# Kernel optimization log

Measured on AMD Instinct MI355X. Metric: run time of the kernel, lower is better.

Reference implementation:

```python
import jax, jax.numpy as jnp
import numpy as np

ALPHA = 0.2  # leaky relu negative slope
F_DIM = 128  # n_features


def setup_inputs() -> dict:
    key = jax.random.key(0)
    k1, k2, k3, k4 = jax.random.split(key, 4)
    B, K, F = 4, 256, F_DIM
    E2 = 2 * F  # embed_dim*2 == 2*n_features (embed_dim defaults to n_features)
    x = jax.random.normal(k1, (B, K, F), dtype=jnp.float32)
    # nn.Linear(2F, 2E): weight (out=2E, in=2F), bias (2E,)
    W = jax.random.normal(k2, (E2, 2 * F), dtype=jnp.float32) * np.sqrt(2.0 / (E2 + 2 * F))
    b_lin = jnp.zeros((E2,), dtype=jnp.float32)
    # attention vector a: xavier_uniform with gain 1.414 on shape (2E, 1)
    limit = 1.414 * np.sqrt(6.0 / (E2 + 1))
    a = jax.random.uniform(k3, (E2,), dtype=jnp.float32, minval=-limit, maxval=limit)
    bias = jnp.zeros((K, K), dtype=jnp.float32)
    return {"x": x, "W": W, "b_lin": b_lin, "a": a, "bias": bias}


def reference(x, W, b_lin, a, bias):
    # Faithful math: combined[b,i,j] = cat(x[b,i], x[b,j]); lin is linear, so
    # lin(cat(vi,vj)) = vi @ W1^T + vj @ W2^T + b  with W = [W1 | W2] split on input dim.
    F = x.shape[-1]
    W1, W2 = W[:, :F], W[:, F:]              # each (2E, F)
    s1 = jnp.einsum('bkf,ef->bke', x, W1)     # contribution of the 'query' time step i
    s2 = jnp.einsum('bkf,ef->bke', x, W2)     # contribution of the 'key' time step j
    pre = s1[:, :, None, :] + s2[:, None, :, :] + b_lin  # (B,K,K,2E)
    h = jnp.where(pre >= 0, pre, ALPHA * pre)            # leaky_relu
    e = jnp.einsum('bije,e->bij', h, a) + bias           # (B,K,K)
    attn = jax.nn.softmax(e, axis=2)
    # dropout with train=False is identity (module evaluated in eval mode)
    out = jax.nn.sigmoid(jnp.einsum('bij,bjf->bif', attn, x))  # (B,K,F)
    return out
```

## Files before the change

### kernel.cpp

```cpp
#include <hip/hip_runtime.h>

#define ALPHA 0.2f
constexpr int B  = 4;
constexpr int K  = 256;
constexpr int F  = 128;
constexpr int E2 = 256;
constexpr int ET = 512;

__global__ __launch_bounds__(256) void k1_gemm(const float* __restrict__ x,
                                               const float* __restrict__ W,
                                               const float* __restrict__ bl,
                                               float* __restrict__ S) {
    __shared__ float xt[32][132];
    __shared__ float wt[64][132];
    const int b  = blockIdx.z;
    const int k0 = blockIdx.y * 32;
    const int e0 = blockIdx.x * 64;
    const int tid = threadIdx.x;

    const int col4 = (tid & 31) * 4;
    const int rsub = tid >> 5;
#pragma unroll
    for (int p = 0; p < 4; ++p) {
        int row = p * 8 + rsub;
        *(float4*)&xt[row][col4] =
            *(const float4*)&x[(b * K + k0 + row) * F + col4];
    }
#pragma unroll
    for (int p = 0; p < 8; ++p) {
        int row = p * 8 + rsub;
        int eg  = e0 + row;
        int wr  = eg & (E2 - 1);
        int fb  = (eg >= E2) ? F : 0;
        *(float4*)&wt[row][col4] =
            *(const float4*)&W[wr * (2 * F) + fb + col4];
    }
    __syncthreads();

    const int es = tid & 15;
    const int kb = tid >> 4;
    float acc[2][4] = {};
    for (int f4 = 0; f4 < F; f4 += 4) {
        float4 x0 = *(const float4*)&xt[kb][f4];
        float4 x1 = *(const float4*)&xt[kb + 16][f4];
#pragma unroll
        for (int t = 0; t < 4; ++t) {
            float4 wv = *(const float4*)&wt[es + 16 * t][f4];
            acc[0][t] += x0.x * wv.x + x0.y * wv.y + x0.z * wv.z + x0.w * wv.w;
            acc[1][t] += x1.x * wv.x + x1.y * wv.y + x1.z * wv.z + x1.w * wv.w;
        }
    }

    const bool isS2 = (e0 >= E2);
#pragma unroll
    for (int t = 0; t < 4; ++t) {
        int   eg  = e0 + es + 16 * t;
        float add = isS2 ? bl[eg - E2] : 0.f;
#pragma unroll
        for (int kk = 0; kk < 2; ++kk) {
            int kg = k0 + kb + 16 * kk;
            S[(b * K + kg) * ET + eg] = acc[kk][t] + add;
        }
    }
}

__global__ __launch_bounds__(256) void k2_score(const float* __restrict__ S,
                                                const float* __restrict__ a,
                                                const float* __restrict__ bias,
                                                float* __restrict__ Eo) {
    __shared__ float s1t[16][260];
    __shared__ float s2t[32][260];
    __shared__ float av6[256];
    __shared__ float av4[256];
    const int b  = blockIdx.z;
    const int i0 = blockIdx.y * 16;
    const int j0 = blockIdx.x * 32;
    const int tid = threadIdx.x;

    { float av = a[tid]; av6[tid] = 0.6f * av; av4[tid] = 0.4f * av; }

    const int col4 = (tid & 63) * 4;
    const int rsub = tid >> 6;
#pragma unroll
    for (int p = 0; p < 4; ++p) {
        int row = p * 4 + rsub;
        *(float4*)&s1t[row][col4] =
            *(const float4*)&S[(b * K + i0 + row) * ET + col4];
    }
#pragma unroll
    for (int p = 0; p < 8; ++p) {
        int row = p * 4 + rsub;
        *(float4*)&s2t[row][col4] =
            *(const float4*)&S[(b * K + j0 + row) * ET + E2 + col4];
    }
    __syncthreads();

    const int w    = tid >> 6;
    const int lane = tid & 63;
    const int jl   = lane & 31;
    const int eh   = lane >> 5;
    float acc[4] = {0.f, 0.f, 0.f, 0.f};
    const int ebeg = eh * 128;

#pragma unroll 2
    for (int e = ebeg; e < ebeg + 128; e += 4) {
        float4 sv = *(const float4*)&s2t[jl][e];
        float4 c6 = *(const float4*)&av6[e];
        float4 c4 = *(const float4*)&av4[e];
#pragma unroll
        for (int is = 0; is < 4; ++is) {
            float4 s1v = *(const float4*)&s1t[w * 4 + is][e];
            float p0 = s1v.x + sv.x;
            float p1 = s1v.y + sv.y;
            float p2 = s1v.z + sv.z;
            float p3 = s1v.w + sv.w;
            acc[is] += c6.x * p0 + c4.x * fabsf(p0);
            acc[is] += c6.y * p1 + c4.y * fabsf(p1);
            acc[is] += c6.z * p2 + c4.z * fabsf(p2);
            acc[is] += c6.w * p3 + c4.w * fabsf(p3);
        }
    }
#pragma unroll
    for (int is = 0; is < 4; ++is) acc[is] += __shfl_xor(acc[is], 32);

    if (eh == 0) {
        int jg = j0 + jl;
#pragma unroll
        for (int is = 0; is < 4; ++is) {
            int ig = i0 + w * 4 + is;
            Eo[(b * K + ig) * K + jg] = acc[is] + bias[ig * K + jg];
        }
    }
}

__global__ __launch_bounds__(256) void k3_softmax_pv(const float* __restrict__ Ein,
                                                     const float* __restrict__ x,
                                                     float* __restrict__ out) {
    __shared__ float p_lds[K][4];
    __shared__ float yp[4][4][F];
    __shared__ float rinv_lds[4];
    const int b   = blockIdx.y;
    const int i0  = blockIdx.x * 4;
    const int tid = threadIdx.x;
    const int w   = tid >> 6;
    const int lane = tid & 63;

    const int i = i0 + w;
    const float* Erow = &Ein[(b * K + i) * K];
    float er[4];
#pragma unroll
    for (int m = 0; m < 4; ++m) er[m] = Erow[m * 64 + lane];
    float mx = fmaxf(fmaxf(er[0], er[1]), fmaxf(er[2], er[3]));
#pragma unroll
    for (int off = 32; off > 0; off >>= 1) mx = fmaxf(mx, __shfl_xor(mx, off));
    float pm[4], s = 0.f;
#pragma unroll
    for (int m = 0; m < 4; ++m) { pm[m] = __expf(er[m] - mx); s += pm[m]; }
#pragma unroll
    for (int off = 32; off > 0; off >>= 1) s += __shfl_xor(s, off);
    if (lane == 0) rinv_lds[w] = 1.f / s;
#pragma unroll
    for (int m = 0; m < 4; ++m) p_lds[m * 64 + lane][w] = pm[m];
    __syncthreads();

    float acc[4][2] = {};
    const float* xb = &x[(size_t)(b * K) * F];
#pragma unroll 4
    for (int jj = 0; jj < 64; ++jj) {
        int j = w * 64 + jj;
        float2 xv = *(const float2*)&xb[j * F + lane * 2];
        float4 pj = *(const float4*)&p_lds[j][0];
        acc[0][0] += pj.x * xv.x;  acc[0][1] += pj.x * xv.y;
        acc[1][0] += pj.y * xv.x;  acc[1][1] += pj.y * xv.y;
        acc[2][0] += pj.z * xv.x;  acc[2][1] += pj.z * xv.y;
        acc[3][0] += pj.w * xv.x;  acc[3][1] += pj.w * xv.y;
    }
#pragma unroll
    for (int ii = 0; ii < 4; ++ii) {
        yp[w][ii][lane * 2]     = acc[ii][0];
        yp[w][ii][lane * 2 + 1] = acc[ii][1];
    }
    __syncthreads();

#pragma unroll
    for (int r = 0; r < 2; ++r) {
        int id = r * 256 + tid;
        int ii = id >> 7;
        int f  = id & 127;
        float y = yp[0][ii][f] + yp[1][ii][f] + yp[2][ii][f] + yp[3][ii][f];
        float z = y * rinv_lds[ii];
        out[(b * K + i0 + ii) * F + f] = 1.f / (1.f + __expf(-z));
    }
}

extern "C" void kernel_launch(void* const* d_in, const int* in_sizes, int n_in,
                              void* d_out, int out_size, void* d_ws, size_t ws_size,
                              hipStream_t stream) {
    const float* x    = (const float*)d_in[0];
    const float* W    = (const float*)d_in[1];
    const float* bl   = (const float*)d_in[2];
    const float* a    = (const float*)d_in[3];
    const float* bias = (const float*)d_in[4];
    float* out = (float*)d_out;

    float* S = (float*)d_ws;
    float* E = (float*)((char*)d_ws + (size_t)B * K * ET * sizeof(float));

    k1_gemm      <<<dim3(ET / 64, K / 32, B), 256, 0, stream>>>(x, W, bl, S);
    k2_score     <<<dim3(K / 32, K / 16, B), 256, 0, stream>>>(S, a, bias, E);
    k3_softmax_pv<<<dim3(K / 4, B),          256, 0, stream>>>(E, x, out);
}
```

Before: 29.29 us.

## Fuse score computation with softmax and PV, shrink GEMM tile for more blocks

The score kernel and the softmax/PV kernel are merged, so each block of 4 query rows computes its full 256-wide score row in registers and LDS, streaming S2 tiles through double-buffered shared memory. This removes the intermediate E buffer round trip through global memory and one kernel launch. The GEMM tile along E is halved so the first kernel launches twice as many blocks. In exchange, each fused block rereads all of S2 for its batch, and per-block LDS grows (about 90 KB), which limits occupancy. The fused grid is only 256 blocks.

Result: slower. 36.90 us (+26.0%).

```diff
diff --git a/kernel.cpp b/kernel.cpp
--- a/kernel.cpp
+++ b/kernel.cpp
@@ -1,6 +1,5 @@
 #include <hip/hip_runtime.h>
 
-#define ALPHA 0.2f
 constexpr int B  = 4;
 constexpr int K  = 256;
 constexpr int F  = 128;
@@ -12,10 +11,10 @@
                                                const float* __restrict__ bl,
                                                float* __restrict__ S) {
     __shared__ float xt[32][132];
-    __shared__ float wt[64][132];
+    __shared__ float wt[32][132];
     const int b  = blockIdx.z;
     const int k0 = blockIdx.y * 32;
-    const int e0 = blockIdx.x * 64;
+    const int e0 = blockIdx.x * 32;
     const int tid = threadIdx.x;
 
     const int col4 = (tid & 31) * 4;
@@ -25,13 +24,9 @@
         int row = p * 8 + rsub;
         *(float4*)&xt[row][col4] =
             *(const float4*)&x[(b * K + k0 + row) * F + col4];
-    }
-#pragma unroll
-    for (int p = 0; p < 8; ++p) {
-        int row = p * 8 + rsub;
-        int eg  = e0 + row;
-        int wr  = eg & (E2 - 1);
-        int fb  = (eg >= E2) ? F : 0;
+        int eg = e0 + row;
+        int wr = eg & (E2 - 1);
+        int fb = (eg >= E2) ? F : 0;
         *(float4*)&wt[row][col4] =
             *(const float4*)&W[wr * (2 * F) + fb + col4];
     }
@@ -39,128 +34,136 @@
 
     const int es = tid & 15;
     const int kb = tid >> 4;
-    float acc[2][4] = {};
+    float acc[2][2] = {};
     for (int f4 = 0; f4 < F; f4 += 4) {
         float4 x0 = *(const float4*)&xt[kb][f4];
         float4 x1 = *(const float4*)&xt[kb + 16][f4];
-#pragma unroll
-        for (int t = 0; t < 4; ++t) {
-            float4 wv = *(const float4*)&wt[es + 16 * t][f4];
-            acc[0][t] += x0.x * wv.x + x0.y * wv.y + x0.z * wv.z + x0.w * wv.w;
-            acc[1][t] += x1.x * wv.x + x1.y * wv.y + x1.z * wv.z + x1.w * wv.w;
-        }
+        float4 w0 = *(const float4*)&wt[es][f4];
+        float4 w1 = *(const float4*)&wt[es + 16][f4];
+        acc[0][0] += x0.x * w0.x + x0.y * w0.y + x0.z * w0.z + x0.w * w0.w;
+        acc[0][1] += x0.x * w1.x + x0.y * w1.y + x0.z * w1.z + x0.w * w1.w;
+        acc[1][0] += x1.x * w0.x + x1.y * w0.y + x1.z * w0.z + x1.w * w0.w;
+        acc[1][1] += x1.x * w1.x + x1.y * w1.y + x1.z * w1.z + x1.w * w1.w;
     }
 
     const bool isS2 = (e0 >= E2);
 #pragma unroll
-    for (int t = 0; t < 4; ++t) {
+    for (int t = 0; t < 2; ++t) {
         int   eg  = e0 + es + 16 * t;
         float add = isS2 ? bl[eg - E2] : 0.f;
-#pragma unroll
-        for (int kk = 0; kk < 2; ++kk) {
-            int kg = k0 + kb + 16 * kk;
-            S[(b * K + kg) * ET + eg] = acc[kk][t] + add;
-        }
+        S[(b * K + k0 + kb) * ET + eg]      = acc[0][t] + add;
+        S[(b * K + k0 + kb + 16) * ET + eg] = acc[1][t] + add;
     }
 }
 
-__global__ __launch_bounds__(256) void k2_score(const float* __restrict__ S,
+__global__ __launch_bounds__(256) void kb_fused(const float* __restrict__ S,
+                                                const float* __restrict__ x,
                                                 const float* __restrict__ a,
                                                 const float* __restrict__ bias,
-                                                float* __restrict__ Eo) {
-    __shared__ float s1t[16][260];
-    __shared__ float s2t[32][260];
-    __shared__ float av6[256];
-    __shared__ float av4[256];
-    const int b  = blockIdx.z;
-    const int i0 = blockIdx.y * 16;
-    const int j0 = blockIdx.x * 32;
-    const int tid = threadIdx.x;
-
-    { float av = a[tid]; av6[tid] = 0.6f * av; av4[tid] = 0.4f * av; }
-
-    const int col4 = (tid & 63) * 4;
-    const int rsub = tid >> 6;
-#pragma unroll
-    for (int p = 0; p < 4; ++p) {
-        int row = p * 4 + rsub;
-        *(float4*)&s1t[row][col4] =
-            *(const float4*)&S[(b * K + i0 + row) * ET + col4];
-    }
-#pragma unroll
-    for (int p = 0; p < 8; ++p) {
-        int row = p * 4 + rsub;
-        *(float4*)&s2t[row][col4] =
-            *(const float4*)&S[(b * K + j0 + row) * ET + E2 + col4];
-    }
-    __syncthreads();
-
+                                                float* __restrict__ out) {
+    __shared__ float s2t[2][32][260];
+    __shared__ float s1t[4][260];
+    __shared__ float av6[E2], av4[E2];
+    __shared__ float scp[4][4][K];
+    __shared__ float p_lds[K][4];
+    __shared__ float yp[4][4][F];
+    __shared__ float rinv_lds[4];
+    const int b    = blockIdx.y;
+    const int i0   = blockIdx.x * 4;
+    const int tid  = threadIdx.x;
     const int w    = tid >> 6;
     const int lane = tid & 63;
     const int jl   = lane & 31;
     const int eh   = lane >> 5;
-    float acc[4] = {0.f, 0.f, 0.f, 0.f};
-    const int ebeg = eh * 128;
-
-#pragma unroll 2
-    for (int e = ebeg; e < ebeg + 128; e += 4) {
-        float4 sv = *(const float4*)&s2t[jl][e];
-        float4 c6 = *(const float4*)&av6[e];
-        float4 c4 = *(const float4*)&av4[e];
-#pragma unroll
-        for (int is = 0; is < 4; ++is) {
-            float4 s1v = *(const float4*)&s1t[w * 4 + is][e];
-            float p0 = s1v.x + sv.x;
-            float p1 = s1v.y + sv.y;
-            float p2 = s1v.z + sv.z;
-            float p3 = s1v.w + sv.w;
-            acc[is] += c6.x * p0 + c4.x * fabsf(p0);
-            acc[is] += c6.y * p1 + c4.y * fabsf(p1);
-            acc[is] += c6.z * p2 + c4.z * fabsf(p2);
-            acc[is] += c6.w * p3 + c4.w * fabsf(p3);
+
+    { float av = a[tid]; av6[tid] = 0.6f * av; av4[tid] = 0.4f * av; }
+    {
+        int row = tid >> 6, c4 = (tid & 63) * 4;
+        *(float4*)&s1t[row][c4] =
+            *(const float4*)&S[(b * K + i0 + row) * ET + c4];
+    }
+#pragma unroll
+    for (int p = 0; p < 8; ++p) {
+        int idx = p * 256 + tid;
+        int row = idx >> 6, c4 = (idx & 63) * 4;
+        *(float4*)&s2t[0][row][c4] =
+            *(const float4*)&S[(b * K + row) * ET + E2 + c4];
+    }
+    __syncthreads();
+
+    float er[4][8];
+    const int eb = w * 64 + eh * 32;
+#pragma unroll
+    for (int jt = 0; jt < 8; ++jt) {
+        const int cur = jt & 1;
+        if (jt < 7) {
+            int j0n = (jt + 1) * 32;
+#pragma unroll
+            for (int p = 0; p < 8; ++p) {
+                int idx = p * 256 + tid;
+                int row = idx >> 6, c4 = (idx & 63) * 4;
+                *(float4*)&s2t[cur ^ 1][row][c4] =
+                    *(const float4*)&S[(b * K + j0n + row) * ET + E2 + c4];
+            }
         }
-    }
-#pragma unroll
-    for (int is = 0; is < 4; ++is) acc[is] += __shfl_xor(acc[is], 32);
-
+        float ac[4] = {0.f, 0.f, 0.f, 0.f};
+#pragma unroll
+        for (int m = 0; m < 8; ++m) {
+            const int e = eb + m * 4;
+            float4 sv  = *(const float4*)&s2t[cur][jl][e];
+            float4 c6  = *(const float4*)&av6[e];
+            float4 c4v = *(const float4*)&av4[e];
+#pragma unroll
+            for (int is = 0; is < 4; ++is) {
+                float4 s1v = *(const float4*)&s1t[is][e];
+                float p0 = s1v.x + sv.x;
+                float p1 = s1v.y + sv.y;
+                float p2 = s1v.z + sv.z;
+                float p3 = s1v.w + sv.w;
+                ac[is] += c6.x * p0 + c4v.x * fabsf(p0);
+                ac[is] += c6.y * p1 + c4v.y * fabsf(p1);
+                ac[is] += c6.z * p2 + c4v.z * fabsf(p2);
+                ac[is] += c6.w * p3 + c4v.w * fabsf(p3);
+            }
+        }
+#pragma unroll
+        for (int is = 0; is < 4; ++is) er[is][jt] = ac[is];
+        __syncthreads();
+    }
+
+#pragma unroll
+    for (int is = 0; is < 4; ++is)
+#pragma unroll
+        for (int jt = 0; jt < 8; ++jt)
+            er[is][jt] += __shfl_xor(er[is][jt], 32);
     if (eh == 0) {
-        int jg = j0 + jl;
-#pragma unroll
-        for (int is = 0; is < 4; ++is) {
-            int ig = i0 + w * 4 + is;
-            Eo[(b * K + ig) * K + jg] = acc[is] + bias[ig * K + jg];
-        }
-    }
-}
-
-__global__ __launch_bounds__(256) void k3_softmax_pv(const float* __restrict__ Ein,
-                                                     const float* __restrict__ x,
-                                                     float* __restrict__ out) {
-    __shared__ float p_lds[K][4];
-    __shared__ float yp[4][4][F];
-    __shared__ float rinv_lds[4];
-    const int b   = blockIdx.y;
-    const int i0  = blockIdx.x * 4;
-    const int tid = threadIdx.x;
-    const int w   = tid >> 6;
-    const int lane = tid & 63;
+#pragma unroll
+        for (int is = 0; is < 4; ++is)
+#pragma unroll
+            for (int jt = 0; jt < 8; ++jt)
+                scp[w][is][jt * 32 + jl] = er[is][jt];
+    }
+    __syncthreads();
 
     const int i = i0 + w;
-    const float* Erow = &Ein[(b * K + i) * K];
-    float er[4];
-#pragma unroll
-    for (int m = 0; m < 4; ++m) er[m] = Erow[m * 64 + lane];
-    float mx = fmaxf(fmaxf(er[0], er[1]), fmaxf(er[2], er[3]));
+    float sc[4];
+#pragma unroll
+    for (int mm = 0; mm < 4; ++mm) {
+        int j = mm * 64 + lane;
+        sc[mm] = scp[0][w][j] + scp[1][w][j] + scp[2][w][j] + scp[3][w][j]
+               + bias[i * K + j];
+    }
+    float mx = fmaxf(fmaxf(sc[0], sc[1]), fmaxf(sc[2], sc[3]));
 #pragma unroll
     for (int off = 32; off > 0; off >>= 1) mx = fmaxf(mx, __shfl_xor(mx, off));
-    float pm[4], s = 0.f;
-#pragma unroll
-    for (int m = 0; m < 4; ++m) { pm[m] = __expf(er[m] - mx); s += pm[m]; }
-#pragma unroll
-    for (int off = 32; off > 0; off >>= 1) s += __shfl_xor(s, off);
-    if (lane == 0) rinv_lds[w] = 1.f / s;
-#pragma unroll
-    for (int m = 0; m < 4; ++m) p_lds[m * 64 + lane][w] = pm[m];
+    float pm[4], ssum = 0.f;
+#pragma unroll
+    for (int mm = 0; mm < 4; ++mm) { pm[mm] = __expf(sc[mm] - mx); ssum += pm[mm]; }
+#pragma unroll
+    for (int off = 32; off > 0; off >>= 1) ssum += __shfl_xor(ssum, off);
+    if (lane == 0) rinv_lds[w] = 1.f / ssum;
+#pragma unroll
+    for (int mm = 0; mm < 4; ++mm) p_lds[mm * 64 + lane][w] = pm[mm];
     __syncthreads();
 
     float acc[4][2] = {};
@@ -204,9 +207,7 @@
     float* out = (float*)d_out;
 
     float* S = (float*)d_ws;
-    float* E = (float*)((char*)d_ws + (size_t)B * K * ET * sizeof(float));
-
-    k1_gemm      <<<dim3(ET / 64, K / 32, B), 256, 0, stream>>>(x, W, bl, S);
-    k2_score     <<<dim3(K / 32, K / 16, B), 256, 0, stream>>>(S, a, bias, E);
-    k3_softmax_pv<<<dim3(K / 4, B),          256, 0, stream>>>(E, x, out);
+
+    k1_gemm <<<dim3(ET / 32, K / 32, B), 256, 0, stream>>>(x, W, bl, S);
+    kb_fused<<<dim3(K / 4, B),           256, 0, stream>>>(S, x, a, bias, out);
 }
```

## Drop row-constant score term and register-block the score kernel over keys

Applied to the files above, without the earlier changes.

The score kernel rewrites leaky ReLU as 0.6p + 0.4|p| and drops the a·s1 term, which is constant along the softmax axis and so cancels in the softmax. The linear a·s2 term is computed once per key column. Each lane now holds one key's S2 slice and the scaled attention vector in registers, reads query rows from LDS as broadcasts, and the four waves' partial sums over the embedding dimension are reduced through shared memory. The GEMM kernel's output tile is halved to 32 columns, which doubles its block count. Costs are higher register pressure from 128 floats of per-lane arrays, and the intermediate scores now differ from the reference by a row constant.

Measured after the change: 31.38 us. 1.07x slower.

```diff
diff --git a/kernel.cpp b/kernel.cpp
--- a/kernel.cpp
+++ b/kernel.cpp
@@ -1,6 +1,5 @@
 #include <hip/hip_runtime.h>
 
-#define ALPHA 0.2f
 constexpr int B  = 4;
 constexpr int K  = 256;
 constexpr int F  = 128;
@@ -12,10 +11,10 @@
                                                const float* __restrict__ bl,
                                                float* __restrict__ S) {
     __shared__ float xt[32][132];
-    __shared__ float wt[64][132];
+    __shared__ float wt[32][132];
     const int b  = blockIdx.z;
     const int k0 = blockIdx.y * 32;
-    const int e0 = blockIdx.x * 64;
+    const int e0 = blockIdx.x * 32;
     const int tid = threadIdx.x;
 
     const int col4 = (tid & 31) * 4;
@@ -25,13 +24,9 @@
         int row = p * 8 + rsub;
         *(float4*)&xt[row][col4] =
             *(const float4*)&x[(b * K + k0 + row) * F + col4];
-    }
-#pragma unroll
-    for (int p = 0; p < 8; ++p) {
-        int row = p * 8 + rsub;
-        int eg  = e0 + row;
-        int wr  = eg & (E2 - 1);
-        int fb  = (eg >= E2) ? F : 0;
+        int eg = e0 + row;
+        int wr = eg & (E2 - 1);
+        int fb = (eg >= E2) ? F : 0;
         *(float4*)&wt[row][col4] =
             *(const float4*)&W[wr * (2 * F) + fb + col4];
     }
@@ -39,28 +34,25 @@
 
     const int es = tid & 15;
     const int kb = tid >> 4;
-    float acc[2][4] = {};
+    float acc[2][2] = {};
     for (int f4 = 0; f4 < F; f4 += 4) {
         float4 x0 = *(const float4*)&xt[kb][f4];
         float4 x1 = *(const float4*)&xt[kb + 16][f4];
-#pragma unroll
-        for (int t = 0; t < 4; ++t) {
-            float4 wv = *(const float4*)&wt[es + 16 * t][f4];
-            acc[0][t] += x0.x * wv.x + x0.y * wv.y + x0.z * wv.z + x0.w * wv.w;
-            acc[1][t] += x1.x * wv.x + x1.y * wv.y + x1.z * wv.z + x1.w * wv.w;
-        }
+        float4 w0 = *(const float4*)&wt[es][f4];
+        float4 w1 = *(const float4*)&wt[es + 16][f4];
+        acc[0][0] += x0.x * w0.x + x0.y * w0.y + x0.z * w0.z + x0.w * w0.w;
+        acc[0][1] += x0.x * w1.x + x0.y * w1.y + x0.z * w1.z + x0.w * w1.w;
+        acc[1][0] += x1.x * w0.x + x1.y * w0.y + x1.z * w0.z + x1.w * w0.w;
+        acc[1][1] += x1.x * w1.x + x1.y * w1.y + x1.z * w1.z + x1.w * w1.w;
     }
 
     const bool isS2 = (e0 >= E2);
 #pragma unroll
-    for (int t = 0; t < 4; ++t) {
+    for (int t = 0; t < 2; ++t) {
         int   eg  = e0 + es + 16 * t;
         float add = isS2 ? bl[eg - E2] : 0.f;
-#pragma unroll
-        for (int kk = 0; kk < 2; ++kk) {
-            int kg = k0 + kb + 16 * kk;
-            S[(b * K + kg) * ET + eg] = acc[kk][t] + add;
-        }
+        S[(b * K + k0 + kb) * ET + eg]      = acc[0][t] + add;
+        S[(b * K + k0 + kb + 16) * ET + eg] = acc[1][t] + add;
     }
 }
 
@@ -68,68 +60,72 @@
                                                 const float* __restrict__ a,
                                                 const float* __restrict__ bias,
                                                 float* __restrict__ Eo) {
-    __shared__ float s1t[16][260];
-    __shared__ float s2t[32][260];
-    __shared__ float av6[256];
-    __shared__ float av4[256];
-    const int b  = blockIdx.z;
-    const int i0 = blockIdx.y * 16;
-    const int j0 = blockIdx.x * 32;
-    const int tid = threadIdx.x;
-
-    { float av = a[tid]; av6[tid] = 0.6f * av; av4[tid] = 0.4f * av; }
-
-    const int col4 = (tid & 63) * 4;
-    const int rsub = tid >> 6;
-#pragma unroll
-    for (int p = 0; p < 4; ++p) {
-        int row = p * 4 + rsub;
-        *(float4*)&s1t[row][col4] =
-            *(const float4*)&S[(b * K + i0 + row) * ET + col4];
-    }
-#pragma unroll
-    for (int p = 0; p < 8; ++p) {
-        int row = p * 4 + rsub;
-        *(float4*)&s2t[row][col4] =
-            *(const float4*)&S[(b * K + j0 + row) * ET + E2 + col4];
-    }
-    __syncthreads();
-
+    __shared__ float s1t[8][256];
+    __shared__ float scp[4][8][64];
+    __shared__ float vp[4][64];
+    const int b    = blockIdx.z;
+    const int i0   = blockIdx.y * 8;
+    const int j0   = blockIdx.x * 64;
+    const int tid  = threadIdx.x;
     const int w    = tid >> 6;
     const int lane = tid & 63;
-    const int jl   = lane & 31;
-    const int eh   = lane >> 5;
-    float acc[4] = {0.f, 0.f, 0.f, 0.f};
-    const int ebeg = eh * 128;
-
-#pragma unroll 2
-    for (int e = ebeg; e < ebeg + 128; e += 4) {
-        float4 sv = *(const float4*)&s2t[jl][e];
-        float4 c6 = *(const float4*)&av6[e];
-        float4 c4 = *(const float4*)&av4[e];
-#pragma unroll
-        for (int is = 0; is < 4; ++is) {
-            float4 s1v = *(const float4*)&s1t[w * 4 + is][e];
-            float p0 = s1v.x + sv.x;
-            float p1 = s1v.y + sv.y;
-            float p2 = s1v.z + sv.z;
-            float p3 = s1v.w + sv.w;
-            acc[is] += c6.x * p0 + c4.x * fabsf(p0);
-            acc[is] += c6.y * p1 + c4.y * fabsf(p1);
-            acc[is] += c6.z * p2 + c4.z * fabsf(p2);
-            acc[is] += c6.w * p3 + c4.w * fabsf(p3);
+    const int e0   = w * 64;
+
+#pragma unroll
+    for (int p = 0; p < 2; ++p) {
+        int id = p * 256 + tid;
+        int row = id >> 6, c4 = (id & 63) * 4;
+        *(float4*)&s1t[row][c4] =
+            *(const float4*)&S[(b * K + i0 + row) * ET + c4];
+    }
+
+    float a4r[64], s2r[64];
+    {
+        const float* s2p = &S[((size_t)(b * K + j0 + lane)) * ET + E2 + e0];
+#pragma unroll
+        for (int m = 0; m < 16; ++m) {
+            float4 av = *(const float4*)&a[e0 + m * 4];
+            float4 sv = *(const float4*)&s2p[m * 4];
+            a4r[m * 4 + 0] = 0.4f * av.x;  s2r[m * 4 + 0] = sv.x;
+            a4r[m * 4 + 1] = 0.4f * av.y;  s2r[m * 4 + 1] = sv.y;
+            a4r[m * 4 + 2] = 0.4f * av.z;  s2r[m * 4 + 2] = sv.z;
+            a4r[m * 4 + 3] = 0.4f * av.w;  s2r[m * 4 + 3] = sv.w;
         }
     }
-#pragma unroll
-    for (int is = 0; is < 4; ++is) acc[is] += __shfl_xor(acc[is], 32);
-
-    if (eh == 0) {
-        int jg = j0 + jl;
-#pragma unroll
-        for (int is = 0; is < 4; ++is) {
-            int ig = i0 + w * 4 + is;
-            Eo[(b * K + ig) * K + jg] = acc[is] + bias[ig * K + jg];
+    float vpt = 0.f;
+#pragma unroll
+    for (int e = 0; e < 64; ++e) vpt = fmaf(a4r[e], s2r[e], vpt);
+    vp[w][lane] = vpt;
+    __syncthreads();
+
+#pragma unroll
+    for (int ii = 0; ii < 8; ++ii) {
+        float a0 = 0.f, a1 = 0.f;
+#pragma unroll
+        for (int m = 0; m < 16; ++m) {
+            float4 s1v = *(const float4*)&s1t[ii][e0 + m * 4];
+            float t0 = s2r[m * 4 + 0] + s1v.x;
+            float t1 = s2r[m * 4 + 1] + s1v.y;
+            float t2 = s2r[m * 4 + 2] + s1v.z;
+            float t3 = s2r[m * 4 + 3] + s1v.w;
+            a0 = fmaf(a4r[m * 4 + 0], fabsf(t0), a0);
+            a1 = fmaf(a4r[m * 4 + 1], fabsf(t1), a1);
+            a0 = fmaf(a4r[m * 4 + 2], fabsf(t2), a0);
+            a1 = fmaf(a4r[m * 4 + 3], fabsf(t3), a1);
         }
+        scp[w][ii][lane] = a0 + a1;
+    }
+    __syncthreads();
+
+#pragma unroll
+    for (int r = 0; r < 2; ++r) {
+        int id = r * 256 + tid;
+        int ii = id >> 6, jl = id & 63;
+        float s = scp[0][ii][jl] + scp[1][ii][jl]
+                + scp[2][ii][jl] + scp[3][ii][jl];
+        float v = 1.5f * (vp[0][jl] + vp[1][jl] + vp[2][jl] + vp[3][jl]);
+        int ig = i0 + ii, jg = j0 + jl;
+        Eo[(b * K + ig) * K + jg] = s + v + bias[ig * K + jg];
     }
 }
 
@@ -206,7 +202,7 @@
     float* S = (float*)d_ws;
     float* E = (float*)((char*)d_ws + (size_t)B * K * ET * sizeof(float));
 
-    k1_gemm      <<<dim3(ET / 64, K / 32, B), 256, 0, stream>>>(x, W, bl, S);
-    k2_score     <<<dim3(K / 32, K / 16, B), 256, 0, stream>>>(S, a, bias, E);
+    k1_gemm     <<<dim3(ET / 32, K / 32, B), 256, 0, stream>>>(x, W, bl, S);
+    k2_score    <<<dim3(K / 64, K / 8, B),   256, 0, stream>>>(S, a, bias, E);
     k3_softmax_pv<<<dim3(K / 4, B),          256, 0, stream>>>(E, x, out);
 }
```

## Fuse score computation with softmax and PV into a single kernel

Applied to the files above, without the earlier changes.

Merges the score kernel and the softmax/PV kernel into one kernel, one block per 4 query rows, so the intermediate score matrix no longer goes through global memory. The leaky-relu dot product is split algebraically into a linear term (0.6·a·s1 + 0.6·a·s2) and an |·| term. The s1 part is constant per row and cancels in the softmax, and the s2 part is computed once per j. s2 tiles are streamed through a double-buffered LDS pipeline. The cost is only 256 blocks, each iterating serially over all 256 keys with heavy register use, which lowers parallelism compared with the earlier wide score grid.

New measurement: 29.23 us. Within noise of the previous version (-0.2%).

```diff
diff --git a/kernel.cpp b/kernel.cpp
--- a/kernel.cpp
+++ b/kernel.cpp
@@ -1,13 +1,12 @@
 #include <hip/hip_runtime.h>
 
-#define ALPHA 0.2f
 constexpr int B  = 4;
 constexpr int K  = 256;
 constexpr int F  = 128;
 constexpr int E2 = 256;
 constexpr int ET = 512;
 
-__global__ __launch_bounds__(256) void k1_gemm(const float* __restrict__ x,
+__global__ __launch_bounds__(256) void kA_gemm(const float* __restrict__ x,
                                                const float* __restrict__ W,
                                                const float* __restrict__ bl,
                                                float* __restrict__ S) {
@@ -64,101 +63,127 @@
     }
 }
 
-__global__ __launch_bounds__(256) void k2_score(const float* __restrict__ S,
-                                                const float* __restrict__ a,
-                                                const float* __restrict__ bias,
-                                                float* __restrict__ Eo) {
-    __shared__ float s1t[16][260];
-    __shared__ float s2t[32][260];
-    __shared__ float av6[256];
-    __shared__ float av4[256];
-    const int b  = blockIdx.z;
-    const int i0 = blockIdx.y * 16;
-    const int j0 = blockIdx.x * 32;
-    const int tid = threadIdx.x;
-
-    { float av = a[tid]; av6[tid] = 0.6f * av; av4[tid] = 0.4f * av; }
-
-    const int col4 = (tid & 63) * 4;
-    const int rsub = tid >> 6;
-#pragma unroll
-    for (int p = 0; p < 4; ++p) {
-        int row = p * 4 + rsub;
-        *(float4*)&s1t[row][col4] =
-            *(const float4*)&S[(b * K + i0 + row) * ET + col4];
-    }
-#pragma unroll
-    for (int p = 0; p < 8; ++p) {
-        int row = p * 4 + rsub;
-        *(float4*)&s2t[row][col4] =
-            *(const float4*)&S[(b * K + j0 + row) * ET + E2 + col4];
-    }
-    __syncthreads();
-
+__global__ __launch_bounds__(256, 1) void kB_fused(const float* __restrict__ S,
+                                                   const float* __restrict__ x,
+                                                   const float* __restrict__ a,
+                                                   const float* __restrict__ bias,
+                                                   float* __restrict__ out) {
+    __shared__ float s2t[2][32][260];
+    __shared__ float s1t[4][260];
+    __shared__ float scp[4][4][K];
+    __shared__ float vp[4][K];
+    __shared__ float p_lds[K][4];
+    __shared__ float yp[4][4][F];
+    __shared__ float rinv_lds[4];
+    const int tid  = threadIdx.x;
+    const int blk  = blockIdx.x;
+    const int b    = blk >> 6;
+    const int i0   = (blk & 63) * 4;
     const int w    = tid >> 6;
     const int lane = tid & 63;
     const int jl   = lane & 31;
     const int eh   = lane >> 5;
-    float acc[4] = {0.f, 0.f, 0.f, 0.f};
-    const int ebeg = eh * 128;
-
-#pragma unroll 2
-    for (int e = ebeg; e < ebeg + 128; e += 4) {
-        float4 sv = *(const float4*)&s2t[jl][e];
-        float4 c6 = *(const float4*)&av6[e];
-        float4 c4 = *(const float4*)&av4[e];
-#pragma unroll
-        for (int is = 0; is < 4; ++is) {
-            float4 s1v = *(const float4*)&s1t[w * 4 + is][e];
-            float p0 = s1v.x + sv.x;
-            float p1 = s1v.y + sv.y;
-            float p2 = s1v.z + sv.z;
-            float p3 = s1v.w + sv.w;
-            acc[is] += c6.x * p0 + c4.x * fabsf(p0);
-            acc[is] += c6.y * p1 + c4.y * fabsf(p1);
-            acc[is] += c6.z * p2 + c4.z * fabsf(p2);
-            acc[is] += c6.w * p3 + c4.w * fabsf(p3);
-        }
-    }
-#pragma unroll
-    for (int is = 0; is < 4; ++is) acc[is] += __shfl_xor(acc[is], 32);
-
+    const int e0   = w * 64 + eh * 32;
+
+    *(float4*)&s1t[w][lane * 4] =
+        *(const float4*)&S[(b * K + i0 + w) * ET + lane * 4];
+    float4 a4r[8];
+#pragma unroll
+    for (int m = 0; m < 8; ++m) {
+        float4 av = *(const float4*)&a[e0 + m * 4];
+        a4r[m] = make_float4(0.4f * av.x, 0.4f * av.y, 0.4f * av.z, 0.4f * av.w);
+    }
+#pragma unroll
+    for (int p = 0; p < 8; ++p) {
+        int row = p * 4 + w;
+        *(float4*)&s2t[0][row][lane * 4] =
+            *(const float4*)&S[(b * K + row) * ET + E2 + lane * 4];
+    }
+    __syncthreads();
+
+    float er[4][8], vjr[8];
+#pragma unroll
+    for (int t = 0; t < 8; ++t) {
+        const int cur = t & 1;
+        float4 pf[8];
+        if (t < 7) {
+#pragma unroll
+            for (int p = 0; p < 8; ++p) {
+                int row = p * 4 + w;
+                pf[p] = *(const float4*)&S[(b * K + (t + 1) * 32 + row) * ET
+                                           + E2 + lane * 4];
+            }
+        }
+        float4 s2v[8];
+#pragma unroll
+        for (int m = 0; m < 8; ++m)
+            s2v[m] = *(const float4*)&s2t[cur][jl][e0 + m * 4];
+        float vt = 0.f;
+#pragma unroll
+        for (int m = 0; m < 8; ++m) {
+            vt = fmaf(a4r[m].x, s2v[m].x, vt);
+            vt = fmaf(a4r[m].y, s2v[m].y, vt);
+            vt = fmaf(a4r[m].z, s2v[m].z, vt);
+            vt = fmaf(a4r[m].w, s2v[m].w, vt);
+        }
+        vjr[t] = vt;
+#pragma unroll
+        for (int i = 0; i < 4; ++i) {
+            float acc = 0.f;
+#pragma unroll
+            for (int m = 0; m < 8; ++m) {
+                float4 s1v = *(const float4*)&s1t[i][e0 + m * 4];
+                acc = fmaf(a4r[m].x, fabsf(s1v.x + s2v[m].x), acc);
+                acc = fmaf(a4r[m].y, fabsf(s1v.y + s2v[m].y), acc);
+                acc = fmaf(a4r[m].z, fabsf(s1v.z + s2v[m].z), acc);
+                acc = fmaf(a4r[m].w, fabsf(s1v.w + s2v[m].w), acc);
+            }
+            er[i][t] = acc;
+        }
+        if (t < 7) {
+#pragma unroll
+            for (int p = 0; p < 8; ++p) {
+                int row = p * 4 + w;
+                *(float4*)&s2t[cur ^ 1][row][lane * 4] = pf[p];
+            }
+        }
+        __syncthreads();
+    }
+
+#pragma unroll
+    for (int i = 0; i < 4; ++i)
+#pragma unroll
+        for (int t = 0; t < 8; ++t)
+            er[i][t] += __shfl_xor(er[i][t], 32);
+#pragma unroll
+    for (int t = 0; t < 8; ++t) vjr[t] += __shfl_xor(vjr[t], 32);
     if (eh == 0) {
-        int jg = j0 + jl;
-#pragma unroll
-        for (int is = 0; is < 4; ++is) {
-            int ig = i0 + w * 4 + is;
-            Eo[(b * K + ig) * K + jg] = acc[is] + bias[ig * K + jg];
-        }
-    }
-}
-
-__global__ __launch_bounds__(256) void k3_softmax_pv(const float* __restrict__ Ein,
-                                                     const float* __restrict__ x,
-                                                     float* __restrict__ out) {
-    __shared__ float p_lds[K][4];
-    __shared__ float yp[4][4][F];
-    __shared__ float rinv_lds[4];
-    const int b   = blockIdx.y;
-    const int i0  = blockIdx.x * 4;
-    const int tid = threadIdx.x;
-    const int w   = tid >> 6;
-    const int lane = tid & 63;
-
-    const int i = i0 + w;
-    const float* Erow = &Ein[(b * K + i) * K];
-    float er[4];
-#pragma unroll
-    for (int m = 0; m < 4; ++m) er[m] = Erow[m * 64 + lane];
-    float mx = fmaxf(fmaxf(er[0], er[1]), fmaxf(er[2], er[3]));
-#pragma unroll
-    for (int off = 32; off > 0; off >>= 1) mx = fmaxf(mx, __shfl_xor(mx, off));
-    float pm[4], s = 0.f;
-#pragma unroll
-    for (int m = 0; m < 4; ++m) { pm[m] = __expf(er[m] - mx); s += pm[m]; }
-#pragma unroll
-    for (int off = 32; off > 0; off >>= 1) s += __shfl_xor(s, off);
-    if (lane == 0) rinv_lds[w] = 1.f / s;
+#pragma unroll
+        for (int t = 0; t < 8; ++t) {
+            vp[w][t * 32 + jl] = vjr[t];
+#pragma unroll
+            for (int i = 0; i < 4; ++i) scp[w][i][t * 32 + jl] = er[i][t];
+        }
+    }
+    __syncthreads();
+
+    float sc[4];
+#pragma unroll
+    for (int m = 0; m < 4; ++m) {
+        int j = m * 64 + lane;
+        sc[m] = scp[0][w][j] + scp[1][w][j] + scp[2][w][j] + scp[3][w][j]
+              + 1.5f * (vp[0][j] + vp[1][j] + vp[2][j] + vp[3][j])
+              + bias[(i0 + w) * K + j];
+    }
+    float mx = fmaxf(fmaxf(sc[0], sc[1]), fmaxf(sc[2], sc[3]));
+#pragma unroll
+    for (int off = 32; off; off >>= 1) mx = fmaxf(mx, __shfl_xor(mx, off));
+    float pm[4], ssum = 0.f;
+#pragma unroll
+    for (int m = 0; m < 4; ++m) { pm[m] = __expf(sc[m] - mx); ssum += pm[m]; }
+#pragma unroll
+    for (int off = 32; off; off >>= 1) ssum += __shfl_xor(ssum, off);
+    if (lane == 0) rinv_lds[w] = 1.f / ssum;
 #pragma unroll
     for (int m = 0; m < 4; ++m) p_lds[m * 64 + lane][w] = pm[m];
     __syncthreads();
@@ -167,13 +192,13 @@
     const float* xb = &x[(size_t)(b * K) * F];
 #pragma unroll 4
     for (int jj = 0; jj < 64; ++jj) {
-        int j = w * 64 + jj;
-        float2 xv = *(const float2*)&xb[j * F + lane * 2];
-        float4 pj = *(const float4*)&p_lds[j][0];
-        acc[0][0] += pj.x * xv.x;  acc[0][1] += pj.x * xv.y;
-        acc[1][0] += pj.y * xv.x;  acc[1][1] += pj.y * xv.y;
-        acc[2][0] += pj.z * xv.x;  acc[2][1] += pj.z * xv.y;
-        acc[3][0] += pj.w * xv.x;  acc[3][1] += pj.w * xv.y;
+        int jq = w * 64 + jj;
+        float2 xv = *(const float2*)&xb[jq * F + lane * 2];
+        float4 pj = *(const float4*)&p_lds[jq][0];
+        acc[0][0] = fmaf(pj.x, xv.x, acc[0][0]);  acc[0][1] = fmaf(pj.x, xv.y, acc[0][1]);
+        acc[1][0] = fmaf(pj.y, xv.x, acc[1][0]);  acc[1][1] = fmaf(pj.y, xv.y, acc[1][1]);
+        acc[2][0] = fmaf(pj.z, xv.x, acc[2][0]);  acc[2][1] = fmaf(pj.z, xv.y, acc[2][1]);
+        acc[3][0] = fmaf(pj.w, xv.x, acc[3][0]);  acc[3][1] = fmaf(pj.w, xv.y, acc[3][1]);
     }
 #pragma unroll
     for (int ii = 0; ii < 4; ++ii) {
@@ -188,8 +213,8 @@
         int ii = id >> 7;
         int f  = id & 127;
         float y = yp[0][ii][f] + yp[1][ii][f] + yp[2][ii][f] + yp[3][ii][f];
-        float z = y * rinv_lds[ii];
-        out[(b * K + i0 + ii) * F + f] = 1.f / (1.f + __expf(-z));
+        out[(b * K + i0 + ii) * F + f] =
+            1.f / (1.f + __expf(-y * rinv_lds[ii]));
     }
 }
 
@@ -202,11 +227,8 @@
     const float* a    = (const float*)d_in[3];
     const float* bias = (const float*)d_in[4];
     float* out = (float*)d_out;
-
-    float* S = (float*)d_ws;
-    float* E = (float*)((char*)d_ws + (size_t)B * K * ET * sizeof(float));
-
-    k1_gemm      <<<dim3(ET / 64, K / 32, B), 256, 0, stream>>>(x, W, bl, S);
-    k2_score     <<<dim3(K / 32, K / 16, B), 256, 0, stream>>>(S, a, bias, E);
-    k3_softmax_pv<<<dim3(K / 4, B),          256, 0, stream>>>(E, x, out);
+    float* S   = (float*)d_ws;
+
+    kA_gemm <<<dim3(ET / 64, K / 32, B), 256, 0, stream>>>(x, W, bl, S);
+    kB_fused<<<dim3(256),                256, 0, stream>>>(S, x, a, bias, out);
 }
```
